# Kernel tuning notes

Hardware: AMD Instinct MI355X
Metric: run time of the kernel (lower is better)

## Reference

```python
import jax, jax.numpy as jnp
import numpy as np


def setup_inputs() -> dict:
    key = jax.random.key(0)
    k1, k2 = jax.random.split(key)
    x = jax.random.normal(k1, (16, 4096, 256), dtype=jnp.float32)
    embedding = jax.random.normal(k2, (1024, 256), dtype=jnp.float32)
    return {"x": x, "embedding": embedding}


def reference(x, embedding):
    # which_dim = -1 (default): no permute.
    shape = x.shape
    xf = x.reshape(-1, shape[-1])  # [N, D]
    x_sq = jnp.sum(xf * xf, axis=-1, keepdims=True)          # [N, 1]
    e_sq = jnp.sum(embedding * embedding, axis=-1)           # [K]
    dist = -(x_sq - 2.0 * (xf @ embedding.T) + e_sq[None, :])  # [N, K]
    embed_indices = jnp.argmax(dist, axis=1)                 # [N]
    embed_indices = embed_indices.reshape(shape[:-1])        # [B, S]
    quantization = embedding[embed_indices]                  # [B, S, D]
    return (quantization, embed_indices)
```

## Files before the change

### kernel.cpp

```cpp
#include <hip/hip_runtime.h>
#include <hip/hip_fp16.h>
#include <math.h>

#define MROWS   65536
#define NCODES  1024
#define KD      256
#define MARGIN  0.25f

typedef unsigned short u16;
typedef __attribute__((ext_vector_type(8))) _Float16 hfrag;
typedef __attribute__((ext_vector_type(4))) float f32x4;

#define IOFF ((size_t)MROWS * KD)

__device__ __forceinline__ float addrn(float a, float b) {
    float d; asm("v_add_f32 %0, %1, %2" : "=v"(d) : "v"(a), "v"(b)); return d;
}

__device__ __forceinline__ float sumsq_vf8ic4(const float* __restrict__ xr) {
    float a[4][8];
#pragma unroll
    for (int i = 0; i < 4; ++i)
#pragma unroll
        for (int l = 0; l < 8; ++l) a[i][l] = 0.f;
#pragma unroll
    for (int m = 0; m < 8; ++m)
#pragma unroll
        for (int i = 0; i < 4; ++i)
#pragma unroll
            for (int l = 0; l < 8; ++l) {
                float v = xr[m * 32 + i * 8 + l];
                a[i][l] = fmaf(v, v, a[i][l]);
            }
    float cc[8];
#pragma unroll
    for (int l = 0; l < 8; ++l)
        cc[l] = addrn(addrn(addrn(a[0][l], a[1][l]), a[2][l]), a[3][l]);
    float u0 = addrn(cc[0], cc[4]), u1 = addrn(cc[1], cc[5]);
    float u2 = addrn(cc[2], cc[6]), u3 = addrn(cc[3], cc[7]);
    return addrn(addrn(u0, u2), addrn(u1, u3));
}

__global__ __launch_bounds__(256)
void vq_pack(const float* __restrict__ src, u16* __restrict__ dh,
             unsigned int* __restrict__ cnt) {
    if (blockIdx.x == 0 && threadIdx.x == 0) *cnt = 0;
    __shared__ __align__(16) float lx[16 * 260];
    const int t = threadIdx.x;
    const size_t base = (size_t)blockIdx.x * 16 * 256;
#pragma unroll
    for (int qq = 0; qq < 4; ++qq) {
        int i4 = qq * 256 + t;
        int row = i4 >> 6, col = (i4 & 63) * 4;
        *(float4*)(lx + row * 260 + col) = *(const float4*)(src + base + (size_t)i4 * 4);
    }
    __syncthreads();
#pragma unroll
    for (int i = 0; i < 2; ++i) {
        int s = t + 256 * i;
        int kb = s >> 6, lane = s & 63;
        int r = lane & 15, kg = lane >> 4;
        int k0 = kb * 32 + kg * 8;
        u16 vh[8];
#pragma unroll
        for (int j = 0; j < 8; ++j) {
            float v = lx[r * 260 + k0 + j];
            vh[j] = __half_as_ushort(__float2half(v));
        }
        size_t off = (((size_t)blockIdx.x * 8 + kb) * 64 + lane) * 8;
        *(ulonglong2*)(dh + off) = *(ulonglong2*)vh;
    }
}

__global__ __launch_bounds__(256)
void vq_prep_emb(const float* __restrict__ emb, u16* __restrict__ Eh,
                 float* __restrict__ esq, float* __restrict__ embT) {
    __shared__ float lx[64 * 257];
    const int t = threadIdx.x;
    const int c0 = blockIdx.x * 64;
    const size_t base = (size_t)c0 * 256;
#pragma unroll
    for (int qq = 0; qq < 16; ++qq) {
        int idx4 = qq * 256 + t;
        int row = idx4 >> 6, col4 = idx4 & 63;
        *(float4*)(lx + row * 257 + col4 * 4) = *(const float4*)(emb + base + (size_t)idx4 * 4);
    }
    __syncthreads();
    if (t < 64) esq[c0 + t] = sumsq_vf8ic4(lx + t * 257);
#pragma unroll
    for (int i = 0; i < 8; ++i) {
        int s = i * 256 + t;
        int fl = s >> 6, lane = s & 63;
        int rb_l = fl >> 3, kb = fl & 7;
        int g = blockIdx.x * 4 + rb_l;
        int p = g >> 3, gg = g & 7;
        int wn = gg >> 2, ni = gg & 3;
        int frag = (p * 8 + kb) * 8 + wn * 4 + ni;
        int r = rb_l * 16 + (lane & 15), kg = lane >> 4;
        int k0 = kb * 32 + kg * 8;
        u16 vh[8];
#pragma unroll
        for (int j = 0; j < 8; ++j)
            vh[j] = __half_as_ushort(__float2half(lx[r * 257 + k0 + j]));
        size_t off = ((size_t)frag * 64 + lane) * 8;
        *(ulonglong2*)(Eh + off) = *(ulonglong2*)vh;
    }
#pragma unroll
    for (int i = 0; i < 64; ++i) {
        int k = i * 4 + (t >> 6), col = t & 63;
        embT[(size_t)k * 1024 + c0 + col] = lx[col * 257 + k];
    }
}

__global__ __launch_bounds__(256, 2)
void vq_gemm(const u16* __restrict__ Ah, const u16* __restrict__ Eh,
             const float* __restrict__ esq, float* __restrict__ tw) {
    __shared__ u16 ldsA[32 * 512];
    const int t = threadIdx.x;
    const int wave = t >> 6, lane = t & 63;
    const int wm = wave >> 1, wn = wave & 1;
    const int q = lane >> 4, c = lane & 15;
    const int m0 = blockIdx.x * 64;

#pragma unroll
    for (int u = 0; u < 8; ++u) {
        int f = wave * 8 + u;
        const u16* srcp = Ah + ((size_t)(blockIdx.x * 32 + f) * 64 + lane) * 8;
        __builtin_amdgcn_global_load_lds((const unsigned int*)srcp,
                                         (unsigned int*)(ldsA + f * 512), 16, 0, 0);
    }
    __syncthreads();

    const u16* pB = Eh + (size_t)wn * 2048 + (size_t)lane * 8;
    const char* aB = (const char*)ldsA + wm * 16384 + lane * 16;

    float b1[8], s2v[8], bi[8];
#pragma unroll
    for (int r = 0; r < 8; ++r) { b1[r] = INFINITY; s2v[r] = INFINITY; bi[r] = 0.f; }

    f32x4 acc[2][4];
#pragma unroll
    for (int mi = 0; mi < 2; ++mi)
#pragma unroll
        for (int ni = 0; ni < 4; ++ni) acc[mi][ni] = 0.f;

    hfrag bA[4], bB[4];
#pragma unroll
    for (int ni = 0; ni < 4; ++ni) bA[ni] = *(const hfrag*)(pB + 0 * 4096 + ni * 512);
#pragma unroll
    for (int ni = 0; ni < 4; ++ni) bB[ni] = *(const hfrag*)(pB + 1 * 4096 + ni * 512);

    for (int p = 0; p < 8; ++p) {
        const u16* pPp = pB + (size_t)p * 32768;
#pragma unroll
        for (int ks = 0; ks < 8; ++ks) {
            hfrag af0 = *(const hfrag*)(aB + 0 * 8192 + ks * 1024);
            hfrag af1 = *(const hfrag*)(aB + 1 * 8192 + ks * 1024);
            if ((ks & 1) == 0) {
#pragma unroll
                for (int ni = 0; ni < 4; ++ni) {
                    acc[0][ni] = __builtin_amdgcn_mfma_f32_16x16x32_f16(af0, bA[ni], acc[0][ni], 0, 0, 0);
                    acc[1][ni] = __builtin_amdgcn_mfma_f32_16x16x32_f16(af1, bA[ni], acc[1][ni], 0, 0, 0);
                }
#pragma unroll
                for (int ni = 0; ni < 4; ++ni)
                    bA[ni] = *(const hfrag*)(pPp + (ks + 2) * 4096 + ni * 512);
            } else {
#pragma unroll
                for (int ni = 0; ni < 4; ++ni) {
                    acc[0][ni] = __builtin_amdgcn_mfma_f32_16x16x32_f16(af0, bB[ni], acc[0][ni], 0, 0, 0);
                    acc[1][ni] = __builtin_amdgcn_mfma_f32_16x16x32_f16(af1, bB[ni], acc[1][ni], 0, 0, 0);
                }
#pragma unroll
                for (int ni = 0; ni < 4; ++ni)
                    bB[ni] = *(const hfrag*)(pPp + (ks + 2) * 4096 + ni * 512);
            }
        }
#pragma unroll
        for (int ni = 0; ni < 4; ++ni) {
            const int code = p * 128 + wn * 64 + ni * 16 + c;
            const float e2 = esq[code];
            const float ci = (float)code;
#pragma unroll
            for (int mi = 0; mi < 2; ++mi)
#pragma unroll
                for (int j = 0; j < 4; ++j) {
                    const int r = mi * 4 + j;
                    float sc = fmaf(-2.f, acc[mi][ni][j], e2);
                    bool lt = sc < b1[r];
                    s2v[r] = fminf(s2v[r], lt ? b1[r] : sc);
                    if (lt) { b1[r] = sc; bi[r] = ci; }
                }
        }
#pragma unroll
        for (int mi = 0; mi < 2; ++mi)
#pragma unroll
            for (int ni = 0; ni < 4; ++ni) acc[mi][ni] = 0.f;
    }

#pragma unroll
    for (int r = 0; r < 8; ++r) {
#pragma unroll
        for (int mm = 1; mm < 16; mm <<= 1) {
            float ob = __shfl_xor(b1[r], mm, 64);
            float os = __shfl_xor(s2v[r], mm, 64);
            float oi = __shfl_xor(bi[r], mm, 64);
            if (ob < b1[r]) { s2v[r] = fminf(b1[r], os); b1[r] = ob; bi[r] = oi; }
            else            { s2v[r] = fminf(s2v[r], ob); }
        }
    }
    __syncthreads();
    float* sm = (float*)ldsA;
    if (c == 0) {
#pragma unroll
        for (int mi = 0; mi < 2; ++mi)
#pragma unroll
            for (int j = 0; j < 4; ++j) {
                int r = mi * 4 + j;
                int row_l = wm * 32 + mi * 16 + q * 4 + j;
                sm[row_l * 6 + wn * 3 + 0] = b1[r];
                sm[row_l * 6 + wn * 3 + 1] = s2v[r];
                sm[row_l * 6 + wn * 3 + 2] = bi[r];
            }
    }
    __syncthreads();
    if (t < 64) {
        float b0 = sm[t * 6 + 0], s0 = sm[t * 6 + 1], i0 = sm[t * 6 + 2];
        float bb = sm[t * 6 + 3], s1 = sm[t * 6 + 4], i1 = sm[t * 6 + 5];
        float b, s2, bidx;
        if (b0 <= bb) { b = b0; bidx = i0; s2 = fminf(s0, bb); }
        else          { b = bb; bidx = i1; s2 = fminf(s1, b0); }
        size_t row = (size_t)(m0 + t);
        tw[row * 4 + 0] = b;
        tw[row * 4 + 1] = s2;
        tw[row * 4 + 2] = bidx;
    }
}

__global__ __launch_bounds__(256)
void vq_flag_gather(const float* __restrict__ tw, const float* __restrict__ emb,
                    float* __restrict__ idxf, float* __restrict__ quant,
                    unsigned int* __restrict__ cnt, int* __restrict__ list) {
    __shared__ int idx_l[64];
    const int t = threadIdx.x;
    const int r0 = blockIdx.x * 64;
    if (t < 64) {
        int row = r0 + t;
        float b  = tw[(size_t)row * 4 + 0];
        float s2 = tw[(size_t)row * 4 + 1];
        int bidx = (int)tw[(size_t)row * 4 + 2];
        idxf[row] = (float)bidx;
        idx_l[t] = bidx;
        if (s2 - b < MARGIN) {
            unsigned int pos = atomicAdd(cnt, 1u);
            list[pos] = row;
        }
    }
    __syncthreads();
    const int lane = t & 63, w = t >> 6;
#pragma unroll
    for (int u = 0; u < 16; ++u) {
        int rl = u * 4 + w;
        int idx = idx_l[rl];
        *(float4*)(quant + (size_t)(r0 + rl) * 256 + lane * 4) =
            *(const float4*)(emb + (size_t)idx * 256 + lane * 4);
    }
}

__global__ __launch_bounds__(256)
void vq_refine1(const float* __restrict__ x, const float* __restrict__ emb,
                const float* __restrict__ embT, const float* __restrict__ esq,
                const int* __restrict__ list, const unsigned int* __restrict__ cnt,
                float* __restrict__ idxf, float* __restrict__ quant) {
    __shared__ __align__(16) float xs[8][260];
    __shared__ float xsq_s[8];
    __shared__ float lb[8][4];
    __shared__ int   li[8][4];
    __shared__ int   li2[8];
    const int t = threadIdx.x;
    const int wave = t >> 6, lane = t & 63;
    const unsigned int n = *cnt;
    float e2q[4];
#pragma unroll
    for (int qq = 0; qq < 4; ++qq) e2q[qq] = esq[qq * 256 + t];

    for (unsigned int g = blockIdx.x; g * 8u < n; g += gridDim.x) {
        const unsigned int r0 = g * 8u;
        const int nr = (int)min(8u, n - r0);
        __syncthreads();
#pragma unroll
        for (int u = 0; u < 2; ++u) {
            int s = u * 256 + t;
            int rr = s >> 6, l4 = s & 63;
            if (rr < nr) {
                int row = list[r0 + rr];
                *(float4*)(&xs[rr][l4 * 4]) = *(const float4*)(x + (size_t)row * 256 + l4 * 4);
            }
        }
        __syncthreads();
        if (t < nr) xsq_s[t] = sumsq_vf8ic4(&xs[t][0]);
        __syncthreads();

        float d[8][4];
#pragma unroll
        for (int r = 0; r < 8; ++r)
#pragma unroll
            for (int qq = 0; qq < 4; ++qq) d[r][qq] = 0.f;

        for (int kq = 0; kq < 64; ++kq) {
            float ev[4][4];
#pragma unroll
            for (int j = 0; j < 4; ++j)
#pragma unroll
                for (int qq = 0; qq < 4; ++qq)
                    ev[qq][j] = embT[(size_t)(kq * 4 + j) * 1024 + qq * 256 + t];
            float4 xf[8];
#pragma unroll
            for (int r = 0; r < 8; ++r) xf[r] = *(const float4*)(&xs[r][kq * 4]);
#pragma unroll
            for (int r = 0; r < 8; ++r)
#pragma unroll
                for (int qq = 0; qq < 4; ++qq) {
                    d[r][qq] = fmaf(xf[r].x, ev[qq][0], d[r][qq]);
                    d[r][qq] = fmaf(xf[r].y, ev[qq][1], d[r][qq]);
                    d[r][qq] = fmaf(xf[r].z, ev[qq][2], d[r][qq]);
                    d[r][qq] = fmaf(xf[r].w, ev[qq][3], d[r][qq]);
                }
        }
#pragma unroll
        for (int r = 0; r < 8; ++r) {
            float sv = INFINITY; int bc = 0x7fffffff;
#pragma unroll
            for (int qq = 0; qq < 4; ++qq) {
                float s = addrn(fmaf(-2.f, d[r][qq], xsq_s[r]), e2q[qq]);
                if (s < sv) { sv = s; bc = qq * 256 + t; }
            }
#pragma unroll
            for (int mm = 1; mm < 64; mm <<= 1) {
                float ob = __shfl_xor(sv, mm, 64);
                int oi = __shfl_xor(bc, mm, 64);
                if (ob < sv || (ob == sv && oi < bc)) { sv = ob; bc = oi; }
            }
            if (lane == 0) { lb[r][wave] = sv; li[r][wave] = bc; }
        }
        __syncthreads();
        if (t < nr) {
            float best = lb[t][0]; int bix = li[t][0];
#pragma unroll
            for (int w = 1; w < 4; ++w) {
                float ob = lb[t][w]; int oi = li[t][w];
                if (ob < best || (ob == best && oi < bix)) { best = ob; bix = oi; }
            }
            idxf[list[r0 + t]] = (float)bix;
            li2[t] = bix;
        }
        __syncthreads();
#pragma unroll
        for (int rr = 0; rr < 2; ++rr) {
            int rl = wave * 2 + rr;
            if (rl < nr) {
                int row = list[r0 + rl];
                int idx = li2[rl];
                *(float4*)(quant + (size_t)row * 256 + lane * 4) =
                    *(const float4*)(emb + (size_t)idx * 256 + lane * 4);
            }
        }
    }
}

extern "C" void kernel_launch(void* const* d_in, const int* in_sizes, int n_in,
                              void* d_out, int out_size, void* d_ws, size_t ws_size,
                              hipStream_t stream) {
    const float* x   = (const float*)d_in[0];
    const float* emb = (const float*)d_in[1];
    float* out  = (float*)d_out;
    float* idxf = out + IOFF;

    u16* Ah = (u16*)out;

    char* ws = (char*)d_ws;
    u16* Eh    = (u16*)(ws);
    float* esq = (float*)(ws + (512 << 10));
    unsigned int* cnt = (unsigned int*)(ws + (640 << 10));
    int* list  = (int*)(ws + (640 << 10) + 256);
    float* embT = (float*)(ws + (1 << 20));
    float* tw   = (float*)(ws + (2 << 20));

    vq_pack<<<dim3(MROWS / 16), dim3(256), 0, stream>>>(x, Ah, cnt);
    vq_prep_emb<<<dim3(16), dim3(256), 0, stream>>>(emb, Eh, esq, embT);
    vq_gemm<<<dim3(MROWS / 64), dim3(256), 0, stream>>>(Ah, Eh, esq, tw);
    vq_flag_gather<<<dim3(MROWS / 64), dim3(256), 0, stream>>>(tw, emb, idxf, out, cnt, list);
    vq_refine1<<<dim3(512), dim3(256), 0, stream>>>(x, emb, embT, esq, list, cnt, idxf, out);
}
```

Baseline: 146.0 us.

## Fuse x fp16 packing into GEMM and double rows per block

Removes the separate vq_pack kernel. The GEMM now loads fp32 x directly, converts it to fp16 and stores the fragment layout in LDS. Each block now covers 128 rows instead of 64 (4x4 MFMA tiles per wave), and the B fragments rotate through four register buffers for deeper prefetch. This drops a full write and reread of the packed activations plus one launch, and reuses each B fragment across more rows. In exchange it uses more registers and LDS per block, which may lower occupancy, and the in-kernel conversion may expose global load latency.

Result: slower. 154.1 us (+5.5%).

```diff
diff --git a/kernel.cpp b/kernel.cpp
--- a/kernel.cpp
+++ b/kernel.cpp
@@ -42,39 +42,10 @@
 }
 
 __global__ __launch_bounds__(256)
-void vq_pack(const float* __restrict__ src, u16* __restrict__ dh,
-             unsigned int* __restrict__ cnt) {
+void vq_prep_emb(const float* __restrict__ emb, u16* __restrict__ Eh,
+                 float* __restrict__ esq, float* __restrict__ embT,
+                 unsigned int* __restrict__ cnt) {
     if (blockIdx.x == 0 && threadIdx.x == 0) *cnt = 0;
-    __shared__ __align__(16) float lx[16 * 260];
-    const int t = threadIdx.x;
-    const size_t base = (size_t)blockIdx.x * 16 * 256;
-#pragma unroll
-    for (int qq = 0; qq < 4; ++qq) {
-        int i4 = qq * 256 + t;
-        int row = i4 >> 6, col = (i4 & 63) * 4;
-        *(float4*)(lx + row * 260 + col) = *(const float4*)(src + base + (size_t)i4 * 4);
-    }
-    __syncthreads();
-#pragma unroll
-    for (int i = 0; i < 2; ++i) {
-        int s = t + 256 * i;
-        int kb = s >> 6, lane = s & 63;
-        int r = lane & 15, kg = lane >> 4;
-        int k0 = kb * 32 + kg * 8;
-        u16 vh[8];
-#pragma unroll
-        for (int j = 0; j < 8; ++j) {
-            float v = lx[r * 260 + k0 + j];
-            vh[j] = __half_as_ushort(__float2half(v));
-        }
-        size_t off = (((size_t)blockIdx.x * 8 + kb) * 64 + lane) * 8;
-        *(ulonglong2*)(dh + off) = *(ulonglong2*)vh;
-    }
-}
-
-__global__ __launch_bounds__(256)
-void vq_prep_emb(const float* __restrict__ emb, u16* __restrict__ Eh,
-                 float* __restrict__ esq, float* __restrict__ embT) {
     __shared__ float lx[64 * 257];
     const int t = threadIdx.x;
     const int c0 = blockIdx.x * 64;
@@ -113,76 +84,78 @@
 }
 
 __global__ __launch_bounds__(256, 2)
-void vq_gemm(const u16* __restrict__ Ah, const u16* __restrict__ Eh,
+void vq_gemm(const float* __restrict__ x, const u16* __restrict__ Eh,
              const float* __restrict__ esq, float* __restrict__ tw) {
-    __shared__ u16 ldsA[32 * 512];
+    __shared__ u16 ldsA[64 * 512];
     const int t = threadIdx.x;
     const int wave = t >> 6, lane = t & 63;
     const int wm = wave >> 1, wn = wave & 1;
     const int q = lane >> 4, c = lane & 15;
-    const int m0 = blockIdx.x * 64;
-
-#pragma unroll
-    for (int u = 0; u < 8; ++u) {
-        int f = wave * 8 + u;
-        const u16* srcp = Ah + ((size_t)(blockIdx.x * 32 + f) * 64 + lane) * 8;
-        __builtin_amdgcn_global_load_lds((const unsigned int*)srcp,
-                                         (unsigned int*)(ldsA + f * 512), 16, 0, 0);
-    }
-    __syncthreads();
-
-    const u16* pB = Eh + (size_t)wn * 2048 + (size_t)lane * 8;
-    const char* aB = (const char*)ldsA + wm * 16384 + lane * 16;
-
-    float b1[8], s2v[8], bi[8];
-#pragma unroll
-    for (int r = 0; r < 8; ++r) { b1[r] = INFINITY; s2v[r] = INFINITY; bi[r] = 0.f; }
-
-    f32x4 acc[2][4];
-#pragma unroll
-    for (int mi = 0; mi < 2; ++mi)
+    const int m0 = blockIdx.x * 128;
+
+#pragma unroll 4
+    for (int u = 0; u < 32; ++u) {
+        int i4 = u * 256 + t;
+        int row = i4 >> 6, c4 = i4 & 63;
+        float4 v = *(const float4*)(x + (size_t)(m0 + row) * 256 + c4 * 4);
+        int ccol = c4 * 4;
+        int kb = ccol >> 5, kg = (ccol >> 3) & 3, j0 = ccol & 7;
+        int lp = (row & 15) + 16 * kg;
+        int frag = (row >> 4) * 8 + kb;
+        u16 h[4] = { __half_as_ushort(__float2half(v.x)),
+                     __half_as_ushort(__float2half(v.y)),
+                     __half_as_ushort(__float2half(v.z)),
+                     __half_as_ushort(__float2half(v.w)) };
+        *(unsigned long long*)((char*)ldsA + frag * 1024 + lp * 16 + j0 * 2) =
+            *(unsigned long long*)h;
+    }
+    __syncthreads();
+
+    const u16* pB = Eh + wn * 2048 + (size_t)lane * 8;
+
+    float b1[16], s2v[16], bi[16];
+#pragma unroll
+    for (int r = 0; r < 16; ++r) { b1[r] = INFINITY; s2v[r] = INFINITY; bi[r] = 0.f; }
+
+    f32x4 acc[4][4];
+#pragma unroll
+    for (int mi = 0; mi < 4; ++mi)
 #pragma unroll
         for (int ni = 0; ni < 4; ++ni) acc[mi][ni] = 0.f;
 
-    hfrag bA[4], bB[4];
-#pragma unroll
-    for (int ni = 0; ni < 4; ++ni) bA[ni] = *(const hfrag*)(pB + 0 * 4096 + ni * 512);
-#pragma unroll
-    for (int ni = 0; ni < 4; ++ni) bB[ni] = *(const hfrag*)(pB + 1 * 4096 + ni * 512);
+    auto LB = [&](int s, hfrag (&bf)[4]) {
+#pragma unroll
+        for (int ni = 0; ni < 4; ++ni)
+            bf[ni] = *(const hfrag*)(pB + (size_t)s * 4096 + ni * 512);
+    };
+    auto STEP = [&](int s, hfrag (&bf)[4]) {
+        const int ks = s & 7;
+        hfrag af[4];
+#pragma unroll
+        for (int mi = 0; mi < 4; ++mi)
+            af[mi] = *(const hfrag*)((const char*)ldsA + ((wm * 4 + mi) * 8 + ks) * 1024 + lane * 16);
+#pragma unroll
+        for (int mi = 0; mi < 4; ++mi)
+#pragma unroll
+            for (int ni = 0; ni < 4; ++ni)
+                acc[mi][ni] = __builtin_amdgcn_mfma_f32_16x16x32_f16(af[mi], bf[ni], acc[mi][ni], 0, 0, 0);
+        LB(s + 4, bf);
+    };
+
+    hfrag bu0[4], bu1[4], bu2[4], bu3[4];
+    LB(0, bu0); LB(1, bu1); LB(2, bu2); LB(3, bu3);
 
     for (int p = 0; p < 8; ++p) {
-        const u16* pPp = pB + (size_t)p * 32768;
-#pragma unroll
-        for (int ks = 0; ks < 8; ++ks) {
-            hfrag af0 = *(const hfrag*)(aB + 0 * 8192 + ks * 1024);
-            hfrag af1 = *(const hfrag*)(aB + 1 * 8192 + ks * 1024);
-            if ((ks & 1) == 0) {
-#pragma unroll
-                for (int ni = 0; ni < 4; ++ni) {
-                    acc[0][ni] = __builtin_amdgcn_mfma_f32_16x16x32_f16(af0, bA[ni], acc[0][ni], 0, 0, 0);
-                    acc[1][ni] = __builtin_amdgcn_mfma_f32_16x16x32_f16(af1, bA[ni], acc[1][ni], 0, 0, 0);
-                }
-#pragma unroll
-                for (int ni = 0; ni < 4; ++ni)
-                    bA[ni] = *(const hfrag*)(pPp + (ks + 2) * 4096 + ni * 512);
-            } else {
-#pragma unroll
-                for (int ni = 0; ni < 4; ++ni) {
-                    acc[0][ni] = __builtin_amdgcn_mfma_f32_16x16x32_f16(af0, bB[ni], acc[0][ni], 0, 0, 0);
-                    acc[1][ni] = __builtin_amdgcn_mfma_f32_16x16x32_f16(af1, bB[ni], acc[1][ni], 0, 0, 0);
-                }
-#pragma unroll
-                for (int ni = 0; ni < 4; ++ni)
-                    bB[ni] = *(const hfrag*)(pPp + (ks + 2) * 4096 + ni * 512);
-            }
-        }
+        const int s0 = p * 8;
+        STEP(s0 + 0, bu0); STEP(s0 + 1, bu1); STEP(s0 + 2, bu2); STEP(s0 + 3, bu3);
+        STEP(s0 + 4, bu0); STEP(s0 + 5, bu1); STEP(s0 + 6, bu2); STEP(s0 + 7, bu3);
 #pragma unroll
         for (int ni = 0; ni < 4; ++ni) {
             const int code = p * 128 + wn * 64 + ni * 16 + c;
             const float e2 = esq[code];
             const float ci = (float)code;
 #pragma unroll
-            for (int mi = 0; mi < 2; ++mi)
+            for (int mi = 0; mi < 4; ++mi)
 #pragma unroll
                 for (int j = 0; j < 4; ++j) {
                     const int r = mi * 4 + j;
@@ -193,13 +166,13 @@
                 }
         }
 #pragma unroll
-        for (int mi = 0; mi < 2; ++mi)
+        for (int mi = 0; mi < 4; ++mi)
 #pragma unroll
             for (int ni = 0; ni < 4; ++ni) acc[mi][ni] = 0.f;
     }
 
 #pragma unroll
-    for (int r = 0; r < 8; ++r) {
+    for (int r = 0; r < 16; ++r) {
 #pragma unroll
         for (int mm = 1; mm < 16; mm <<= 1) {
             float ob = __shfl_xor(b1[r], mm, 64);
@@ -213,23 +186,23 @@
     float* sm = (float*)ldsA;
     if (c == 0) {
 #pragma unroll
-        for (int mi = 0; mi < 2; ++mi)
+        for (int mi = 0; mi < 4; ++mi)
 #pragma unroll
             for (int j = 0; j < 4; ++j) {
                 int r = mi * 4 + j;
-                int row_l = wm * 32 + mi * 16 + q * 4 + j;
+                int row_l = wm * 64 + mi * 16 + q * 4 + j;
                 sm[row_l * 6 + wn * 3 + 0] = b1[r];
                 sm[row_l * 6 + wn * 3 + 1] = s2v[r];
                 sm[row_l * 6 + wn * 3 + 2] = bi[r];
             }
     }
     __syncthreads();
-    if (t < 64) {
-        float b0 = sm[t * 6 + 0], s0 = sm[t * 6 + 1], i0 = sm[t * 6 + 2];
-        float bb = sm[t * 6 + 3], s1 = sm[t * 6 + 4], i1 = sm[t * 6 + 5];
+    if (t < 128) {
+        float b0 = sm[t * 6 + 0], sA = sm[t * 6 + 1], i0 = sm[t * 6 + 2];
+        float bb = sm[t * 6 + 3], sB = sm[t * 6 + 4], i1 = sm[t * 6 + 5];
         float b, s2, bidx;
-        if (b0 <= bb) { b = b0; bidx = i0; s2 = fminf(s0, bb); }
-        else          { b = bb; bidx = i1; s2 = fminf(s1, b0); }
+        if (b0 <= bb) { b = b0; bidx = i0; s2 = fminf(sA, bb); }
+        else          { b = bb; bidx = i1; s2 = fminf(sB, b0); }
         size_t row = (size_t)(m0 + t);
         tw[row * 4 + 0] = b;
         tw[row * 4 + 1] = s2;
@@ -376,8 +349,6 @@
     float* out  = (float*)d_out;
     float* idxf = out + IOFF;
 
-    u16* Ah = (u16*)out;
-
     char* ws = (char*)d_ws;
     u16* Eh    = (u16*)(ws);
     float* esq = (float*)(ws + (512 << 10));
@@ -386,9 +357,8 @@
     float* embT = (float*)(ws + (1 << 20));
     float* tw   = (float*)(ws + (2 << 20));
 
-    vq_pack<<<dim3(MROWS / 16), dim3(256), 0, stream>>>(x, Ah, cnt);
-    vq_prep_emb<<<dim3(16), dim3(256), 0, stream>>>(emb, Eh, esq, embT);
-    vq_gemm<<<dim3(MROWS / 64), dim3(256), 0, stream>>>(Ah, Eh, esq, tw);
+    vq_prep_emb<<<dim3(16), dim3(256), 0, stream>>>(emb, Eh, esq, embT, cnt);
+    vq_gemm<<<dim3(MROWS / 128), dim3(256), 0, stream>>>(x, Eh, esq, tw);
     vq_flag_gather<<<dim3(MROWS / 64), dim3(256), 0, stream>>>(tw, emb, idxf, out, cnt, list);
     vq_refine1<<<dim3(512), dim3(256), 0, stream>>>(x, emb, embT, esq, list, cnt, idxf, out);
 }
```
